# Kernel optimization log

Measured on AMD Instinct MI355X. Metric: run time of the kernel, lower is better.

## Reference

```python
import jax, jax.numpy as jnp
import numpy as np


def setup_inputs() -> dict:
    key = jax.random.key(0)
    k1, k2 = jax.random.split(key)
    B, M, L, C, F, K = 8, 32, 1024, 256, 256, 3
    x = jax.random.normal(k1, (B, M, L, C), dtype=jnp.float32)
    W = jax.random.normal(k2, (K, C, F), dtype=jnp.float32) * 0.02  # WIO layout
    b = jnp.zeros((F,), dtype=jnp.float32)
    return {"x": x, "W": W, "b": b}


def reference(x, W, b):
    # Original: tf.map_fn(Conv1D, x) over leading axis of [B, M, L, C].
    # Mathematically identical to one batched 'valid' Conv1D on [B*M, L, C].
    B, M, L, C = x.shape
    K, _, F = W.shape
    xf = x.reshape(B * M, L, C)
    y = jax.lax.conv_general_dilated(
        xf, W,
        window_strides=(1,),
        padding='VALID',
        dimension_numbers=('NWC', 'WIO', 'NWC'),
    ) + b
    return y.reshape(B, M, L - K + 1, F)
```

## Files before the change

kernel.cpp:

```cpp
#include <hip/hip_runtime.h>

typedef __attribute__((ext_vector_type(8))) short short8;
typedef __attribute__((ext_vector_type(4))) float f32x4;

constexpr int L = 1024, C = 256, F = 256;
constexpr int NIMG = 256;
constexpr int LOUT = 1022;
constexpr long MAXROW = (long)NIMG * L - 1;

__device__ inline unsigned short f2bf(float f) {
  union { float f; unsigned u; } v; v.f = f;
  return (unsigned short)((v.u + 0x7FFFu + ((v.u >> 16) & 1u)) >> 16);
}

__device__ inline void g2l16(const unsigned short* g, unsigned short* l) {
  __builtin_amdgcn_global_load_lds(
      (const __attribute__((address_space(1))) unsigned int*)g,
      (__attribute__((address_space(3))) unsigned int*)l, 16, 0, 0);
}

__global__ void wprep(const float* __restrict__ W, unsigned short* __restrict__ Wt) {
  int tid = blockIdx.x * 256 + threadIdx.x;
  int kc = tid >> 8, f = tid & 255;
  int k = kc >> 8, c = kc & 255;
  int slab = c >> 5, kp = c & 31;
  int fh = f >> 7, fp = f & 127;
  Wt[(size_t)((((slab * 3 + k) * 2 + fh) * 128 + fp) * 32 + kp)] = f2bf(W[tid]);
}

__global__ __launch_bounds__(256) void conv_mfma(
    const float* __restrict__ x, const unsigned short* __restrict__ Wt,
    const float* __restrict__ bias, float* __restrict__ y)
{
  __shared__ __align__(16) unsigned short As[130 * 32];
  __shared__ __align__(16) unsigned short Bs[128 * 32];

  const int bid = blockIdx.x;
  const int fh  = bid & 1;
  const int mt  = (bid >> 1) & 7;
  const int img = bid >> 4;
  const int l0  = mt * 128;

  const int tid  = threadIdx.x;
  const int lane = tid & 63;
  const int wv   = tid >> 6;
  const int wr   = wv >> 1;
  const int wc   = wv & 1;
  const int lr   = lane & 15;
  const int quad = lane >> 4;

  f32x4 acc[4][4] = {};
  float4 av[2][2];
  float4 avt[2];

  const long gb  = (long)img * L + l0;
  const int  qr  = tid >> 2;
  const int  qc8 = (tid & 3) * 8;

  auto issue_A = [&](int slab) {
    const int cb = slab * 32;
    long g0 = gb + qr;        if (g0 > MAXROW) g0 = MAXROW;
    long g1 = gb + qr + 64;   if (g1 > MAXROW) g1 = MAXROW;
    const float* p0 = x + g0 * C + cb + qc8;
    const float* p1 = x + g1 * C + cb + qc8;
    av[0][0] = *(const float4*)p0; av[0][1] = *(const float4*)(p0 + 4);
    av[1][0] = *(const float4*)p1; av[1][1] = *(const float4*)(p1 + 4);
    if (tid < 8) {
      long g2 = gb + 128 + (tid >> 2); if (g2 > MAXROW) g2 = MAXROW;
      const float* p2 = x + g2 * C + cb + (tid & 3) * 8;
      avt[0] = *(const float4*)p2; avt[1] = *(const float4*)(p2 + 4);
    }
  };

  auto pack8 = [&](float4 a, float4 b) {
    short8 r;
    r[0] = (short)f2bf(a.x); r[1] = (short)f2bf(a.y);
    r[2] = (short)f2bf(a.z); r[3] = (short)f2bf(a.w);
    r[4] = (short)f2bf(b.x); r[5] = (short)f2bf(b.y);
    r[6] = (short)f2bf(b.z); r[7] = (short)f2bf(b.w);
    return r;
  };

  auto write_A = [&]() {
    *(short8*)(As + (size_t)tid * 8)         = pack8(av[0][0], av[0][1]);
    *(short8*)(As + (size_t)(tid + 256) * 8) = pack8(av[1][0], av[1][1]);
    if (tid < 8)
      *(short8*)(As + (size_t)(512 + tid) * 8) = pack8(avt[0], avt[1]);
  };

  issue_A(0);

  for (int slab = 0; slab < 8; ++slab) {
#pragma unroll
    for (int k = 0; k < 3; ++k) {
      __syncthreads();
      if (k == 0) write_A();
      {
        const unsigned short* bsrc = Wt + (size_t)((slab * 3 + k) * 2 + fh) * (128 * 32);
        g2l16(bsrc + (size_t)tid * 8,         Bs + (size_t)tid * 8);
        g2l16(bsrc + (size_t)(tid + 256) * 8, Bs + (size_t)(tid + 256) * 8);
      }
      __syncthreads();

      if (k == 1 && slab < 7) issue_A(slab + 1);

      short8 af[4], bf[4];
#pragma unroll
      for (int mi = 0; mi < 4; ++mi)
        af[mi] = *(const short8*)(As + (wr * 64 + mi * 16 + lr + k) * 32 + quad * 8);
#pragma unroll
      for (int ni = 0; ni < 4; ++ni)
        bf[ni] = *(const short8*)(Bs + (wc * 64 + ni * 16 + lr) * 32 + quad * 8);
#pragma unroll
      for (int mi = 0; mi < 4; ++mi)
#pragma unroll
        for (int ni = 0; ni < 4; ++ni)
          acc[mi][ni] = __builtin_amdgcn_mfma_f32_16x16x32_bf16(af[mi], bf[ni], acc[mi][ni], 0, 0, 0);
    }
  }

  float bv[4];
#pragma unroll
  for (int ni = 0; ni < 4; ++ni)
    bv[ni] = bias[fh * 128 + wc * 64 + ni * 16 + lr];

#pragma unroll
  for (int mi = 0; mi < 4; ++mi) {
#pragma unroll
    for (int r = 0; r < 4; ++r) {
      const int lrow = l0 + wr * 64 + mi * 16 + quad * 4 + r;
      if (lrow < LOUT) {
        float* yp = y + ((size_t)img * LOUT + lrow) * F + fh * 128 + wc * 64 + lr;
#pragma unroll
        for (int ni = 0; ni < 4; ++ni)
          yp[ni * 16] = acc[mi][ni][r] + bv[ni];
      }
    }
  }
}

extern "C" void kernel_launch(void* const* d_in, const int* in_sizes, int n_in,
                              void* d_out, int out_size, void* d_ws, size_t ws_size,
                              hipStream_t stream) {
  const float* x = (const float*)d_in[0];
  const float* W = (const float*)d_in[1];
  const float* b = (const float*)d_in[2];
  float* y = (float*)d_out;
  unsigned short* Wt = (unsigned short*)d_ws;

  wprep<<<768, 256, 0, stream>>>(W, Wt);
  conv_mfma<<<NIMG * 8 * 2, 256, 0, stream>>>(x, Wt, b, y);
}
```

Before: 525.9 us.

## Triple-buffer weight tiles and double-buffer input tiles with manual waitcnt pipelining

Replaces the two-barrier-per-step schedule with a software pipeline. Weight tiles are prefetched two steps ahead into three LDS buffers, and activation slabs are double-buffered. Explicit vmcnt/lgkmcnt waits with a single barrier per step replace __syncthreads, and MFMA sections get raised wave priority. The aim is to hide global load latency behind MFMA work and cut synchronization stalls. The cost is more LDS use and fragile hand-counted waitcnts that could race if the compiler reorders or adds memory ops.

```diff
diff --git a/kernel.cpp b/kernel.cpp
--- a/kernel.cpp
+++ b/kernel.cpp
@@ -32,8 +32,8 @@
     const float* __restrict__ x, const unsigned short* __restrict__ Wt,
     const float* __restrict__ bias, float* __restrict__ y)
 {
-  __shared__ __align__(16) unsigned short As[130 * 32];
-  __shared__ __align__(16) unsigned short Bs[128 * 32];
+  __shared__ __align__(16) unsigned short As[2][130 * 32];
+  __shared__ __align__(16) unsigned short Bs[3][128 * 32];
 
   const int bid = blockIdx.x;
   const int fh  = bid & 1;
@@ -81,41 +81,64 @@
     return r;
   };
 
-  auto write_A = [&]() {
-    *(short8*)(As + (size_t)tid * 8)         = pack8(av[0][0], av[0][1]);
-    *(short8*)(As + (size_t)(tid + 256) * 8) = pack8(av[1][0], av[1][1]);
+  auto write_A = [&](int ab) {
+    *(short8*)(As[ab] + (size_t)tid * 8)         = pack8(av[0][0], av[0][1]);
+    *(short8*)(As[ab] + (size_t)(tid + 256) * 8) = pack8(av[1][0], av[1][1]);
     if (tid < 8)
-      *(short8*)(As + (size_t)(512 + tid) * 8) = pack8(avt[0], avt[1]);
+      *(short8*)(As[ab] + (size_t)(512 + tid) * 8) = pack8(avt[0], avt[1]);
+  };
+
+  auto stage_B = [&](int tile, int bb) {
+    const unsigned short* bsrc = Wt + (size_t)(tile * 2 + fh) * 4096;
+    g2l16(bsrc + (size_t)tid * 8,         Bs[bb] + (size_t)tid * 8);
+    g2l16(bsrc + (size_t)(tid + 256) * 8, Bs[bb] + (size_t)(tid + 256) * 8);
   };
 
   issue_A(0);
+  stage_B(0, 0);
+  stage_B(1, 1);
+  write_A(0);
+  asm volatile("s_waitcnt vmcnt(2) lgkmcnt(0)" ::: "memory");
+  __builtin_amdgcn_s_barrier();
+  __builtin_amdgcn_sched_barrier(0);
 
   for (int slab = 0; slab < 8; ++slab) {
+    const int ab = slab & 1;
 #pragma unroll
     for (int k = 0; k < 3; ++k) {
-      __syncthreads();
-      if (k == 0) write_A();
-      {
-        const unsigned short* bsrc = Wt + (size_t)((slab * 3 + k) * 2 + fh) * (128 * 32);
-        g2l16(bsrc + (size_t)tid * 8,         Bs + (size_t)tid * 8);
-        g2l16(bsrc + (size_t)(tid + 256) * 8, Bs + (size_t)(tid + 256) * 8);
-      }
-      __syncthreads();
-
-      if (k == 1 && slab < 7) issue_A(slab + 1);
+      if (slab < 7 || k == 0)
+        stage_B(slab * 3 + k + 2, (k + 2) % 3);
+      if (k == 0 && slab < 7) issue_A(slab + 1);
 
       short8 af[4], bf[4];
 #pragma unroll
       for (int mi = 0; mi < 4; ++mi)
-        af[mi] = *(const short8*)(As + (wr * 64 + mi * 16 + lr + k) * 32 + quad * 8);
+        af[mi] = *(const short8*)(As[ab] + (wr * 64 + mi * 16 + lr + k) * 32 + quad * 8);
 #pragma unroll
       for (int ni = 0; ni < 4; ++ni)
-        bf[ni] = *(const short8*)(Bs + (wc * 64 + ni * 16 + lr) * 32 + quad * 8);
+        bf[ni] = *(const short8*)(Bs[k] + (wc * 64 + ni * 16 + lr) * 32 + quad * 8);
+
+      if (k == 2 && slab < 7) write_A(ab ^ 1);
+
+      __builtin_amdgcn_s_setprio(1);
 #pragma unroll
       for (int mi = 0; mi < 4; ++mi)
 #pragma unroll
         for (int ni = 0; ni < 4; ++ni)
           acc[mi][ni] = __builtin_amdgcn_mfma_f32_16x16x32_bf16(af[mi], bf[ni], acc[mi][ni], 0, 0, 0);
+      __builtin_amdgcn_s_setprio(0);
+
+      if (slab * 3 + k < 23) {
+        if (slab < 7) {
+          if (k < 2) asm volatile("s_waitcnt vmcnt(6)" ::: "memory");
+          else       asm volatile("s_waitcnt vmcnt(2) lgkmcnt(0)" ::: "memory");
+        } else {
+          if (k == 0) asm volatile("s_waitcnt vmcnt(2)" ::: "memory");
+          else        asm volatile("s_waitcnt vmcnt(0)" ::: "memory");
+        }
+        __builtin_amdgcn_s_barrier();
+        __builtin_amdgcn_sched_barrier(0);
+      }
     }
   }
 
```

Result: faster. 513.6 us (-2.3%).
